# Performance work log

Hardware: AMD Instinct MI355X
Metric: run time of the kernel (lower is better)

## Reference

```python
import jax, jax.numpy as jnp
import numpy as np

B, N_PER_G, DEG = 128, 1024, 8
N = B * N_PER_G
E = N * DEG
IN_DIM, HID, OUT_DIM = 128, 64, 10
EPS = 1e-5


def _gcn(x, src, dst, ew, W, b, n_nodes):
    # GCNConv with add_self_loops=True, symmetric normalization, edge weights ew in {0,1}
    xw = x @ W                                                 # [N, HID]
    deg = jax.ops.segment_sum(ew, dst, num_segments=n_nodes) + 1.0  # +1 self loop
    dinv = jax.lax.rsqrt(deg)
    norm = dinv[src] * dinv[dst] * ew                          # [E]
    agg = jax.ops.segment_sum(xw[src] * norm[:, None], dst, num_segments=n_nodes)
    return agg + xw * (dinv * dinv)[:, None] + b               # self-loop term + bias


def _bn_relu(x, g, beta):
    # BatchNorm1d training-mode stats over node dim (biased var), then ReLU
    mu = x.mean(0)
    var = ((x - mu) ** 2).mean(0)
    return jax.nn.relu((x - mu) * jax.lax.rsqrt(var + EPS) * g + beta)


def _topk_pool(x, src, dst, ew, p, n_per_g):
    # PyG TopKPooling: score = x.p/||p||, keep top ceil(0.8*n) per graph, x *= tanh(score)
    k = (4 * n_per_g + 4) // 5  # ceil(0.8 * n), static
    score = (x @ p) / jnp.linalg.norm(p)                       # [B*n]
    _, idx = jax.lax.top_k(score.reshape(B, n_per_g), k)       # [B, k] local indices
    perm = (idx + (jnp.arange(B) * n_per_g)[:, None]).reshape(-1)  # [B*k] global
    xs = x[perm] * jnp.tanh(score[perm])[:, None]
    # re-index edges; edges touching dropped nodes get weight 0 (mask, fixed E)
    mapping = jnp.full((B * n_per_g,), -1, jnp.int32).at[perm].set(
        jnp.arange(B * k, dtype=jnp.int32))
    ns, nd = mapping[src], mapping[dst]
    valid = (ns >= 0) & (nd >= 0) & (ew > 0)
    return xs, jnp.where(valid, ns, 0), jnp.where(valid, nd, 0), valid.astype(x.dtype), k


def _readout(x, k):
    xg = x.reshape(B, k, HID)
    return jnp.concatenate([xg.mean(1), xg.max(1)], axis=1)    # [B, 2*HID]


def _forward(x, edge_index, W1, b1, gamma1, beta1, p1, W2, b2, gamma2, beta2, p2,
             W3, b3, gamma3, beta3, p3, Wm, bm):
    src, dst = edge_index[0], edge_index[1]
    ew = jnp.ones((E,), x.dtype)
    n = N_PER_G
    blocks = [(W1, b1, gamma1, beta1, p1),
              (W2, b2, gamma2, beta2, p2),
              (W3, b3, gamma3, beta3, p3)]
    readout = jnp.zeros((B, 2 * HID), x.dtype)
    for W, b, g, bt, p in blocks:
        h = _gcn(x, src, dst, ew, W, b, B * n)
        h = _bn_relu(h, g, bt)
        x, src, dst, ew, n = _topk_pool(h, src, dst, ew, p, n)
        readout = readout + _readout(x, n)
    return readout @ Wm + bm                                   # [B, OUT_DIM]


def setup_inputs():
    key = jax.random.key(0)
    ks = jax.random.split(key, 20)
    x = jax.random.normal(ks[0], (N, IN_DIM), jnp.float32)
    src_l = jax.random.randint(ks[1], (E,), 0, N_PER_G)
    dst_l = jax.random.randint(ks[2], (E,), 0, N_PER_G)
    off = jnp.repeat(jnp.arange(B, dtype=jnp.int32) * N_PER_G, N_PER_G * DEG)
    edge_index = jnp.stack([src_l.astype(jnp.int32) + off,
                            dst_l.astype(jnp.int32) + off])   # [2, E] intra-graph
    d = {"x": x, "edge_index": edge_index}
    dims = [(IN_DIM, HID), (HID, HID), (HID, HID)]
    for i, (di, do) in enumerate(dims, 1):
        d[f"W{i}"] = jax.random.normal(ks[3 * i], (di, do), jnp.float32) / np.sqrt(di)
        d[f"b{i}"] = jnp.zeros((do,), jnp.float32)
        d[f"gamma{i}"] = jnp.ones((do,), jnp.float32)
        d[f"beta{i}"] = jnp.zeros((do,), jnp.float32)
        d[f"p{i}"] = jax.random.normal(ks[3 * i + 1], (do,), jnp.float32)
    d["Wm"] = jax.random.normal(ks[15], (2 * HID, OUT_DIM), jnp.float32) / np.sqrt(2 * HID)
    d["bm"] = jnp.zeros((OUT_DIM,), jnp.float32)
    return d


def reference(x, edge_index, W1, b1, gamma1, beta1, p1, W2, b2, gamma2, beta2, p2,
              W3, b3, gamma3, beta3, p3, Wm, bm):
    return _forward(x, edge_index, W1, b1, gamma1, beta1, p1,
                    W2, b2, gamma2, beta2, p2, W3, b3, gamma3, beta3, p3, Wm, bm)
```

## Files before the change

kernel.cpp:

```cpp
#include <hip/hip_runtime.h>
#include <cmath>
#include <cstdint>
#include <cstddef>

#define HID 64
#define NGR 128
#define NTOT 131072
#define EDGES 1048576
#define EPG 8192
#define CPAD 9216
#define SENT 1024

__global__ __launch_bounds__(256) void pack_init(
    const int* __restrict__ ei, uint32_t* __restrict__ packed,
    uint16_t* __restrict__ csr_g, uint32_t* __restrict__ rs_g,
    float* __restrict__ dinv_g, float* __restrict__ sums3,
    float* __restrict__ readout) {
  __shared__ int hist[1024];
  __shared__ int part[256];
  __shared__ int cursor[1024];
  int b = blockIdx.x, t = threadIdx.x;
  for (int i = t; i < 1024; i += 256) hist[i] = 0;
  __syncthreads();
  int ebase = b * EPG, nbase = b << 10;
  for (int e = t; e < EPG; e += 256) {
    uint32_t s = (uint32_t)(ei[ebase + e] - nbase);
    uint32_t d = (uint32_t)(ei[EDGES + ebase + e] - nbase);
    packed[ebase + e] = s | (d << 10);
    atomicAdd(&hist[(int)d], 1);
  }
  __syncthreads();
  int h0 = hist[t * 4], h1 = hist[t * 4 + 1], h2 = hist[t * 4 + 2], h3 = hist[t * 4 + 3];
  int p0 = h0 + (h0 & 1), p1 = h1 + (h1 & 1), p2 = h2 + (h2 & 1), p3 = h3 + (h3 & 1);
  int tot = p0 + p1 + p2 + p3;
  part[t] = tot;
  __syncthreads();
  for (int off = 1; off < 256; off <<= 1) {
    int v = (t >= off) ? part[t - off] : 0;
    __syncthreads();
    part[t] += v;
    __syncthreads();
  }
  int excl = part[t] - tot;
  int r0 = excl, r1 = r0 + p0, r2 = r1 + p1, r3 = r2 + p2;
  cursor[t * 4 + 0] = r0; cursor[t * 4 + 1] = r1;
  cursor[t * 4 + 2] = r2; cursor[t * 4 + 3] = r3;
  uint32_t* rg = rs_g + b * 1025;
  rg[t * 4 + 0] = r0; rg[t * 4 + 1] = r1; rg[t * 4 + 2] = r2; rg[t * 4 + 3] = r3;
  if (t == 255) rg[1024] = part[255];
  for (int i = t; i < 1024; i += 256)
    dinv_g[(b << 10) + i] = rsqrtf((float)hist[i] + 1.0f);
  __syncthreads();
  uint16_t* cg = csr_g + (size_t)b * CPAD;
  for (int e = t; e < EPG; e += 256) {
    uint32_t pk = packed[ebase + e];
    int d = (pk >> 10) & 1023;
    int idx = atomicAdd(&cursor[d], 1);
    cg[idx] = (uint16_t)(pk & 1023);
  }
  __syncthreads();
  for (int d = t; d < 1024; d += 256)
    if (hist[d] & 1) cg[cursor[d]] = (uint16_t)SENT;
  if (b < 3 && t < 128) sums3[b * 128 + t] = 0.0f;
  if (t < 128) readout[b * 128 + t] = 0.0f;
}

template<int DIN>
__global__ __launch_bounds__(256, 4) void gemm_rm(
    const float* __restrict__ X, const float* __restrict__ W,
    float* __restrict__ XWT) {
  __shared__ float sW[DIN * 64];
  const int t = threadIdx.x;
  const int c8 = (t & 7) * 8;
  const int n4 = (t >> 3) * 4;
  const int node0 = blockIdx.x * 128;
#pragma unroll
  for (int i = t; i < DIN * 16; i += 256)
    ((float4*)sW)[i] = ((const float4*)W)[i];
  __syncthreads();

  float acc[4][8];
#pragma unroll
  for (int i = 0; i < 4; i++)
#pragma unroll
    for (int c = 0; c < 8; c++) acc[i][c] = 0.0f;

  const float* xp = X + (size_t)(node0 + n4) * DIN;
#pragma unroll 2
  for (int k0 = 0; k0 < DIN; k0 += 4) {
    float xr[4][4];
#pragma unroll
    for (int i = 0; i < 4; i++) {
      float4 v = *(const float4*)(xp + (size_t)i * DIN + k0);
      xr[i][0] = v.x; xr[i][1] = v.y; xr[i][2] = v.z; xr[i][3] = v.w;
    }
#pragma unroll
    for (int j = 0; j < 4; j++) {
      float4 w0 = *(const float4*)(sW + (k0 + j) * 64 + c8);
      float4 w1 = *(const float4*)(sW + (k0 + j) * 64 + c8 + 4);
      float wn[8] = {w0.x, w0.y, w0.z, w0.w, w1.x, w1.y, w1.z, w1.w};
#pragma unroll
      for (int i = 0; i < 4; i++)
#pragma unroll
        for (int c = 0; c < 8; c++)
          acc[i][c] = fmaf(xr[i][j], wn[c], acc[i][c]);
    }
  }
#pragma unroll
  for (int cc = 0; cc < 8; cc++) {
    float* o = XWT + (size_t)(c8 + cc) * NTOT + node0 + n4;
    *(float4*)o = make_float4(acc[0][cc], acc[1][cc], acc[2][cc], acc[3][cc]);
  }
}

template<int DIN>
__global__ __launch_bounds__(256, 4) void gemm_cm(
    const float* __restrict__ X, const float* __restrict__ W,
    float* __restrict__ XWT) {
  __shared__ float sW[DIN * 64];
  const int t = threadIdx.x;
  const int c8 = (t & 7) * 8;
  const int n4 = (t >> 3) * 4;
  const int node0 = blockIdx.x * 128;
#pragma unroll
  for (int i = t; i < DIN * 16; i += 256)
    ((float4*)sW)[i] = ((const float4*)W)[i];
  __syncthreads();

  float acc[4][8];
#pragma unroll
  for (int i = 0; i < 4; i++)
#pragma unroll
    for (int c = 0; c < 8; c++) acc[i][c] = 0.0f;

  const float* xp = X + node0 + n4;
#pragma unroll 4
  for (int k = 0; k < DIN; k++) {
    float4 xv = *(const float4*)(xp + (size_t)k * NTOT);
    float xr[4] = {xv.x, xv.y, xv.z, xv.w};
    float4 w0 = *(const float4*)(sW + k * 64 + c8);
    float4 w1 = *(const float4*)(sW + k * 64 + c8 + 4);
    float wn[8] = {w0.x, w0.y, w0.z, w0.w, w1.x, w1.y, w1.z, w1.w};
#pragma unroll
    for (int i = 0; i < 4; i++)
#pragma unroll
      for (int c = 0; c < 8; c++)
        acc[i][c] = fmaf(xr[i], wn[c], acc[i][c]);
  }
#pragma unroll
  for (int cc = 0; cc < 8; cc++) {
    float* o = XWT + (size_t)(c8 + cc) * NTOT + node0 + n4;
    *(float4*)o = make_float4(acc[0][cc], acc[1][cc], acc[2][cc], acc[3][cc]);
  }
}

__global__ __launch_bounds__(1024, 8) void edge_agg(
    const uint16_t* __restrict__ csr_g, const uint32_t* __restrict__ rs_g,
    const float* __restrict__ dinv_g, const float* __restrict__ xwT,
    const float* __restrict__ bias, float* __restrict__ hT,
    float* __restrict__ sums) {
  __shared__ float xws[8 * 1028];
  __shared__ float dv[1024];
  __shared__ uint32_t rs[1025];
  __shared__ uint32_t csr_s[CPAD / 2];
  __shared__ float sredS[16][8], sredQ[16][8];
  const int g = blockIdx.x & 127;
  const int q = blockIdx.x >> 7;
  const int c0 = q * 8;
  const int t = threadIdx.x;
  const int gbase = g << 10;

  dv[t] = dinv_g[gbase + t];
  rs[t] = rs_g[g * 1025 + t];
  if (t == 0) rs[1024] = rs_g[g * 1025 + 1024];
  {
    const uint4* src4 = (const uint4*)(csr_g + (size_t)g * CPAD);
    ((uint4*)csr_s)[t] = src4[t];
    if (t < CPAD / 8 - 1024) ((uint4*)csr_s)[1024 + t] = src4[1024 + t];
  }
  for (int slot = t; slot < 2048; slot += 1024) {
    int c = slot >> 8, pos4 = (slot & 255) * 4;
    float4 v = *(const float4*)(xwT + (size_t)(c0 + c) * NTOT + gbase + pos4);
    float4 dd = *(const float4*)(dinv_g + gbase + pos4);
    v.x *= dd.x; v.y *= dd.y; v.z *= dd.z; v.w *= dd.w;
    *(float4*)(xws + c * 1028 + pos4) = v;
  }
  if (t < 32) xws[(t >> 2) * 1028 + 1024 + (t & 3)] = 0.0f;
  __syncthreads();

  const int c = t & 7, j = t >> 3;
  const float* xc = xws + c * 1028;
  const float bv = bias[c0 + c];
  float* hrow = hT + (size_t)(c0 + c) * NTOT + gbase;
  float S = 0.0f, Q = 0.0f;
  for (int d = j; d < 1024; d += 128) {
    float dvd = dv[d];
    if (dvd == 0.0f) continue;
    int e  = rs[d] >> 1;
    int e1 = rs[d + 1] >> 1;
    float a0 = 0.0f, a1 = 0.0f;
    for (; e < e1; e++) {
      uint32_t pk = csr_s[e];
      a0 += xc[pk & 0xFFFFu];
      a1 += xc[pk >> 16];
    }
    float hv = (a0 + a1 + xc[d]) * dvd + bv;
    hrow[d] = hv;
    S += hv; Q += hv * hv;
  }
#pragma unroll
  for (int m = 8; m < 64; m <<= 1) { S += __shfl_xor(S, m); Q += __shfl_xor(Q, m); }
  {
    int lane = t & 63, w = t >> 6;
    if (lane < 8) { sredS[w][lane] = S; sredQ[w][lane] = Q; }
  }
  __syncthreads();
  if (t < 8) {
    float a = 0.0f;
    for (int w2 = 0; w2 < 16; w2++) a += sredS[w2][t];
    atomicAdd(&sums[c0 + t], a);
  } else if (t < 16) {
    int cc = t - 8;
    float a = 0.0f;
    for (int w2 = 0; w2 < 16; w2++) a += sredQ[w2][cc];
    atomicAdd(&sums[64 + cc + c0], a);
  }
}

__global__ __launch_bounds__(256) void score_kernel(
    const float* __restrict__ hT, const float* __restrict__ sums,
    const float* __restrict__ gamma, const float* __restrict__ beta,
    const float* __restrict__ p, const float* __restrict__ dinv_g,
    float* __restrict__ score, float* __restrict__ stanh_g, float inv_n) {
  __shared__ float ssc[64], ssh[64], sp[64];
  __shared__ float sipn;
  int b = blockIdx.x >> 2, seg = (blockIdx.x & 3) << 8;
  int t = threadIdx.x;
  int node = (b << 10) + seg + t;
  if (t < 64) {
    float mu = sums[t] * inv_n;
    float var = fmaxf(sums[64 + t] * inv_n - mu * mu, 0.0f);
    float sc = rsqrtf(var + 1e-5f) * gamma[t];
    ssc[t] = sc; ssh[t] = beta[t] - mu * sc;
    sp[t] = p[t];
  }
  __syncthreads();
  if (t == 0) {
    float s = 0.0f;
    for (int i = 0; i < 64; i++) s += sp[i] * sp[i];
    sipn = rsqrtf(s);
  }
  __syncthreads();
  const float* hp = hT + node;
  float s0 = 0.0f;
#pragma unroll 16
  for (int c = 0; c < 64; c++) {
    float y = fmaxf(fmaf(hp[(size_t)c * NTOT], ssc[c], ssh[c]), 0.0f);
    s0 = fmaf(y, sp[c], s0);
  }
  float v0 = s0 * sipn;
  score[node] = (dinv_g[node] > 0.0f) ? v0 : -INFINITY;
  stanh_g[node] = tanhf(v0);
}

__global__ __launch_bounds__(1024) void topk_kernel(
    const float* __restrict__ score, int* __restrict__ snext_g, int k) {
  __shared__ float __align__(16) ssc2[4 * 260];
  int b = blockIdx.x >> 2, p = blockIdx.x & 3;
  int t = threadIdx.x;
  int gbase = b << 10;
  float sv = score[gbase + t];
  ssc2[(t >> 8) * 260 + (t & 255)] = sv;
  __syncthreads();
  int il = t >> 2, jq = t & 3;
  int gi = p * 256 + il;
  float my = ssc2[(gi >> 8) * 260 + (gi & 255)];
  const float4* base = (const float4*)(ssc2 + jq * 260);
  int jbase = jq * 256;
  int r = 0;
#pragma unroll 8
  for (int m = 0; m < 64; m++) {
    float4 v = base[m];
    int j0 = jbase + m * 4;
    r += (v.x > my) || (v.x == my && (j0 + 0) < gi);
    r += (v.y > my) || (v.y == my && (j0 + 1) < gi);
    r += (v.z > my) || (v.z == my && (j0 + 2) < gi);
    r += (v.w > my) || (v.w == my && (j0 + 3) < gi);
  }
  r += __shfl_xor(r, 1);
  r += __shfl_xor(r, 2);
  if (jq == 0) snext_g[gbase + gi] = (r < k) ? 1 : 0;
}

__global__ __launch_bounds__(256) void pool_kernel(
    const float* __restrict__ hT, const float* __restrict__ sums,
    const float* __restrict__ gamma, const float* __restrict__ beta,
    const float* __restrict__ stanh_g, const int* __restrict__ snext_g,
    const uint16_t* __restrict__ csr_g, const uint32_t* __restrict__ rs_g,
    float* __restrict__ xT_out, float* __restrict__ dinv_g,
    float* __restrict__ readout, int k, float inv_n, int hasNext) {
  __shared__ float ssc[64], ssh[64];
  __shared__ float sth[1024];
  __shared__ int skn[1025];
  __shared__ float redS[4][8], redM[4][8];
  int g = blockIdx.x & 127, q = blockIdx.x >> 7;
  int t = threadIdx.x;
  int gbase = g << 10;
  if (t < 64) {
    float mu = sums[t] * inv_n;
    float var = fmaxf(sums[64 + t] * inv_n - mu * mu, 0.0f);
    float sc = rsqrtf(var + 1e-5f) * gamma[t];
    ssc[t] = sc; ssh[t] = beta[t] - mu * sc;
  }
  for (int i = t; i < 1024; i += 256) {
    sth[i] = stanh_g[gbase + i];
    skn[i] = snext_g[gbase + i];
  }
  if (t == 0) skn[1024] = 0;
  __syncthreads();
  int lane = t & 63, w = t >> 6;
#pragma unroll
  for (int i = 0; i < 8; i++) {
    int c = q * 8 + i;
    const float* hrow = hT + (size_t)c * NTOT + gbase;
    float* xrow = xT_out ? (xT_out + (size_t)c * NTOT + gbase) : nullptr;
    float scc = ssc[c], shh = ssh[c];
    float S = 0.0f, M = -INFINITY;
    for (int nd = t; nd < 1024; nd += 256) {
      bool kn = skn[nd] != 0;
      float y = fmaxf(fmaf(hrow[nd], scc, shh), 0.0f) * sth[nd];
      y = kn ? y : 0.0f;
      if (xrow) xrow[nd] = y;
      S += y;
      if (kn) M = fmaxf(M, y);
    }
#pragma unroll
    for (int m = 1; m < 64; m <<= 1) {
      S += __shfl_xor(S, m);
      M = fmaxf(M, __shfl_xor(M, m));
    }
    if (lane == 0) { redS[w][i] = S; redM[w][i] = M; }
  }
  if (hasNext && t < 128) {
    int d = q * 128 + t;
    if (skn[d]) {
      uint32_t e0 = rs_g[g * 1025 + d], e1 = rs_g[g * 1025 + d + 1];
      const uint16_t* row = csr_g + (size_t)g * CPAD;
      int cnt = 0;
      for (uint32_t e = e0; e < e1; e++) cnt += skn[row[e]];
      dinv_g[gbase + d] = rsqrtf((float)cnt + 1.0f);
    } else {
      dinv_g[gbase + d] = 0.0f;
    }
  }
  __syncthreads();
  if (t < 8) {
    float S = redS[0][t] + redS[1][t] + redS[2][t] + redS[3][t];
    readout[g * 128 + q * 8 + t] += S / (float)k;
  } else if (t < 16) {
    int i = t - 8;
    float M = fmaxf(fmaxf(redM[0][i], redM[1][i]), fmaxf(redM[2][i], redM[3][i]));
    readout[g * 128 + 64 + q * 8 + i] += M;
  }
}

__global__ __launch_bounds__(256) void final_linear(
    const float* __restrict__ readout, const float* __restrict__ Wm,
    const float* __restrict__ bm, float* __restrict__ out) {
  int idx = blockIdx.x * 256 + threadIdx.x;
  if (idx >= NGR * 10) return;
  int b = idx / 10, o = idx - b * 10;
  float acc = bm[o];
  const float* r = readout + (size_t)b * 128;
  for (int c = 0; c < 128; c++) acc = fmaf(r[c], Wm[c * 10 + o], acc);
  out[idx] = acc;
}

extern "C" void kernel_launch(void* const* d_in, const int* in_sizes, int n_in,
                              void* d_out, int out_size, void* d_ws, size_t ws_size,
                              hipStream_t stream) {
  (void)in_sizes; (void)n_in; (void)out_size; (void)ws_size;
  const float* x  = (const float*)d_in[0];
  const int*   ei = (const int*)d_in[1];
  const float* Wk[3]  = {(const float*)d_in[2],  (const float*)d_in[7],  (const float*)d_in[12]};
  const float* bk[3]  = {(const float*)d_in[3],  (const float*)d_in[8],  (const float*)d_in[13]};
  const float* gk[3]  = {(const float*)d_in[4],  (const float*)d_in[9],  (const float*)d_in[14]};
  const float* btk[3] = {(const float*)d_in[5],  (const float*)d_in[10], (const float*)d_in[15]};
  const float* pk[3]  = {(const float*)d_in[6],  (const float*)d_in[11], (const float*)d_in[16]};
  const float* Wm = (const float*)d_in[17];
  const float* bm = (const float*)d_in[18];
  float* out = (float*)d_out;

  float* ws = (float*)d_ws;
  size_t off = 0;
  auto alloc = [&](size_t nfl) {
    float* ptr = ws + off;
    off += (nfl + 63) & ~(size_t)63;
    return ptr;
  };
  float* bufXW = alloc((size_t)NTOT * 64);
  float* bufH  = alloc((size_t)NTOT * 64);
  float* bufX  = alloc((size_t)NTOT * 64);
  float* dinv_g = alloc(NTOT);
  float* score  = alloc(NTOT);
  float* stanh_g = alloc(NTOT);
  int*   snext_g = (int*)alloc(NTOT);
  uint32_t* packed = (uint32_t*)alloc(EDGES);
  uint16_t* csr    = (uint16_t*)alloc((size_t)NGR * CPAD / 2);
  uint32_t* rs     = (uint32_t*)alloc(NGR * 1025);
  float* sums3 = alloc(3 * 128);
  float* readout = alloc(NGR * 2 * HID);

  pack_init<<<NGR, 256, 0, stream>>>(ei, packed, csr, rs, dinv_g, sums3, readout);

  const int   kk[3] = {820, 656, 525};
  const float invn[3] = {1.0f / (float)NTOT, 1.0f / (float)(NGR * 820),
                         1.0f / (float)(NGR * 656)};

  for (int L = 0; L < 3; L++) {
    float* sums = sums3 + L * 128;
    if (L == 0)
      gemm_rm<128><<<NTOT / 128, 256, 0, stream>>>(x, Wk[0], bufXW);
    else
      gemm_cm<64><<<NTOT / 128, 256, 0, stream>>>(bufX, Wk[L], bufXW);
    edge_agg<<<8 * NGR, 1024, 0, stream>>>(csr, rs, dinv_g, bufXW, bk[L], bufH, sums);
    score_kernel<<<4 * NGR, 256, 0, stream>>>(bufH, sums, gk[L], btk[L], pk[L],
                                              dinv_g, score, stanh_g, invn[L]);
    topk_kernel<<<4 * NGR, 1024, 0, stream>>>(score, snext_g, kk[L]);
    pool_kernel<<<8 * NGR, 256, 0, stream>>>(bufH, sums, gk[L], btk[L],
                                             stanh_g, snext_g, csr, rs,
                                             (L < 2) ? bufX : nullptr, dinv_g,
                                             readout, kk[L], invn[L],
                                             (L < 2) ? 1 : 0);
  }
  final_linear<<<5, 256, 0, stream>>>(readout, Wm, bm, out);
}
```

Measured before the change: 498.5 us.

## Fuse score, top-k and pooling into one kernel; apply BN/ReLU/tanh inside next GEMM

Replaces the separate score, topk and pool kernels with one per-graph 1024-thread kernel. It computes scores, ranks them in shared memory, builds the keep mask and tanh multiplier, does the readout reductions and recomputes dinv. The next layer's GEMM now reads the raw aggregated features and applies BN, ReLU and the pooling multiplier on the fly, so the pooled feature buffer is no longer written and re-read. This removes two launches and several global round-trips per layer, but each layer now runs only 128 large blocks for the pooling stage and the GEMM does extra elementwise work per load.

```diff
diff --git a/kernel.cpp b/kernel.cpp
--- a/kernel.cpp
+++ b/kernel.cpp
@@ -86,13 +86,13 @@
     for (int c = 0; c < 8; c++) acc[i][c] = 0.0f;
 
   const float* xp = X + (size_t)(node0 + n4) * DIN;
-#pragma unroll 2
+#pragma unroll 8
   for (int k0 = 0; k0 < DIN; k0 += 4) {
-    float xr[4][4];
+    float x4[4][4];
 #pragma unroll
     for (int i = 0; i < 4; i++) {
       float4 v = *(const float4*)(xp + (size_t)i * DIN + k0);
-      xr[i][0] = v.x; xr[i][1] = v.y; xr[i][2] = v.z; xr[i][3] = v.w;
+      x4[i][0] = v.x; x4[i][1] = v.y; x4[i][2] = v.z; x4[i][3] = v.w;
     }
 #pragma unroll
     for (int j = 0; j < 4; j++) {
@@ -103,21 +103,24 @@
       for (int i = 0; i < 4; i++)
 #pragma unroll
         for (int c = 0; c < 8; c++)
-          acc[i][c] = fmaf(xr[i][j], wn[c], acc[i][c]);
-    }
-  }
-#pragma unroll
-  for (int cc = 0; cc < 8; cc++) {
-    float* o = XWT + (size_t)(c8 + cc) * NTOT + node0 + n4;
-    *(float4*)o = make_float4(acc[0][cc], acc[1][cc], acc[2][cc], acc[3][cc]);
+          acc[i][c] = fmaf(x4[i][j], wn[c], acc[i][c]);
+    }
+  }
+#pragma unroll
+  for (int c = 0; c < 8; c++) {
+    float* o = XWT + (size_t)(c8 + c) * NTOT + node0 + n4;
+    *(float4*)o = make_float4(acc[0][c], acc[1][c], acc[2][c], acc[3][c]);
   }
 }
 
 template<int DIN>
-__global__ __launch_bounds__(256, 4) void gemm_cm(
-    const float* __restrict__ X, const float* __restrict__ W,
-    float* __restrict__ XWT) {
+__global__ __launch_bounds__(256, 4) void gemm_fused(
+    const float* __restrict__ H, const float* __restrict__ sums,
+    const float* __restrict__ gamma, const float* __restrict__ beta,
+    const float* __restrict__ mult_g, const float* __restrict__ W,
+    float* __restrict__ XWT, float inv_n) {
   __shared__ float sW[DIN * 64];
+  __shared__ float ssc[DIN], ssh[DIN];
   const int t = threadIdx.x;
   const int c8 = (t & 7) * 8;
   const int n4 = (t >> 3) * 4;
@@ -125,6 +128,12 @@
 #pragma unroll
   for (int i = t; i < DIN * 16; i += 256)
     ((float4*)sW)[i] = ((const float4*)W)[i];
+  if (t < DIN) {
+    float mu = sums[t] * inv_n;
+    float var = fmaxf(sums[64 + t] * inv_n - mu * mu, 0.0f);
+    float sc = rsqrtf(var + 1e-5f) * gamma[t];
+    ssc[t] = sc; ssh[t] = beta[t] - mu * sc;
+  }
   __syncthreads();
 
   float acc[4][8];
@@ -133,24 +142,30 @@
 #pragma unroll
     for (int c = 0; c < 8; c++) acc[i][c] = 0.0f;
 
-  const float* xp = X + node0 + n4;
-#pragma unroll 4
-  for (int k = 0; k < DIN; k++) {
-    float4 xv = *(const float4*)(xp + (size_t)k * NTOT);
-    float xr[4] = {xv.x, xv.y, xv.z, xv.w};
-    float4 w0 = *(const float4*)(sW + k * 64 + c8);
-    float4 w1 = *(const float4*)(sW + k * 64 + c8 + 4);
+  const float4 m4 = *(const float4*)(mult_g + node0 + n4);
+  const float* hp = H + node0 + n4;
+#pragma unroll 8
+  for (int kk = 0; kk < DIN; kk++) {
+    float4 h4 = *(const float4*)(hp + (size_t)kk * NTOT);
+    float scc = ssc[kk], shh = ssh[kk];
+    float xn[4];
+    xn[0] = fmaxf(fmaf(h4.x, scc, shh), 0.0f) * m4.x;
+    xn[1] = fmaxf(fmaf(h4.y, scc, shh), 0.0f) * m4.y;
+    xn[2] = fmaxf(fmaf(h4.z, scc, shh), 0.0f) * m4.z;
+    xn[3] = fmaxf(fmaf(h4.w, scc, shh), 0.0f) * m4.w;
+    float4 w0 = *(const float4*)(sW + kk * 64 + c8);
+    float4 w1 = *(const float4*)(sW + kk * 64 + c8 + 4);
     float wn[8] = {w0.x, w0.y, w0.z, w0.w, w1.x, w1.y, w1.z, w1.w};
 #pragma unroll
     for (int i = 0; i < 4; i++)
 #pragma unroll
       for (int c = 0; c < 8; c++)
-        acc[i][c] = fmaf(xr[i], wn[c], acc[i][c]);
-  }
-#pragma unroll
-  for (int cc = 0; cc < 8; cc++) {
-    float* o = XWT + (size_t)(c8 + cc) * NTOT + node0 + n4;
-    *(float4*)o = make_float4(acc[0][cc], acc[1][cc], acc[2][cc], acc[3][cc]);
+        acc[i][c] = fmaf(xn[i], wn[c], acc[i][c]);
+  }
+#pragma unroll
+  for (int c = 0; c < 8; c++) {
+    float* o = XWT + (size_t)(c8 + c) * NTOT + node0 + n4;
+    *(float4*)o = make_float4(acc[0][c], acc[1][c], acc[2][c], acc[3][c]);
   }
 }
 
@@ -227,16 +242,23 @@
   }
 }
 
-__global__ __launch_bounds__(256) void score_kernel(
+__global__ __launch_bounds__(1024) void sctp_kernel(
     const float* __restrict__ hT, const float* __restrict__ sums,
     const float* __restrict__ gamma, const float* __restrict__ beta,
-    const float* __restrict__ p, const float* __restrict__ dinv_g,
-    float* __restrict__ score, float* __restrict__ stanh_g, float inv_n) {
+    const float* __restrict__ p,
+    const uint16_t* __restrict__ csr_g, const uint32_t* __restrict__ rs_g,
+    float* __restrict__ dinv_g, float* __restrict__ mult_g,
+    float* __restrict__ readout, int k, float inv_n, int hasNext) {
+  __shared__ float __align__(16) ssc2[4 * 260];
   __shared__ float ssc[64], ssh[64], sp[64];
   __shared__ float sipn;
-  int b = blockIdx.x >> 2, seg = (blockIdx.x & 3) << 8;
-  int t = threadIdx.x;
-  int node = (b << 10) + seg + t;
+  __shared__ float mult_l[1024];
+  __shared__ int skn_l[1025];
+  __shared__ float redS[64], redM[64];
+  const int g = blockIdx.x;
+  const int t = threadIdx.x;
+  const int gbase = g << 10;
+
   if (t < 64) {
     float mu = sums[t] * inv_n;
     float var = fmaxf(sums[64 + t] * inv_n - mu * mu, 0.0f);
@@ -244,6 +266,7 @@
     ssc[t] = sc; ssh[t] = beta[t] - mu * sc;
     sp[t] = p[t];
   }
+  if (t == 1023) skn_l[1024] = 0;
   __syncthreads();
   if (t == 0) {
     float s = 0.0f;
@@ -251,7 +274,8 @@
     sipn = rsqrtf(s);
   }
   __syncthreads();
-  const float* hp = hT + node;
+
+  const float* hp = hT + gbase + t;
   float s0 = 0.0f;
 #pragma unroll 16
   for (int c = 0; c < 64; c++) {
@@ -259,109 +283,70 @@
     s0 = fmaf(y, sp[c], s0);
   }
   float v0 = s0 * sipn;
-  score[node] = (dinv_g[node] > 0.0f) ? v0 : -INFINITY;
-  stanh_g[node] = tanhf(v0);
-}
-
-__global__ __launch_bounds__(1024) void topk_kernel(
-    const float* __restrict__ score, int* __restrict__ snext_g, int k) {
-  __shared__ float __align__(16) ssc2[4 * 260];
-  int b = blockIdx.x >> 2, p = blockIdx.x & 3;
-  int t = threadIdx.x;
-  int gbase = b << 10;
-  float sv = score[gbase + t];
-  ssc2[(t >> 8) * 260 + (t & 255)] = sv;
-  __syncthreads();
-  int il = t >> 2, jq = t & 3;
-  int gi = p * 256 + il;
-  float my = ssc2[(gi >> 8) * 260 + (gi & 255)];
-  const float4* base = (const float4*)(ssc2 + jq * 260);
-  int jbase = jq * 256;
+  float dvv = dinv_g[gbase + t];
+  float my = (dvv > 0.0f) ? v0 : -INFINITY;
+  float th = tanhf(v0);
+  ssc2[(t >> 8) * 260 + (t & 255)] = my;
+  __syncthreads();
+
   int r = 0;
+#pragma unroll
+  for (int q4 = 0; q4 < 4; q4++) {
+    const float4* base = (const float4*)(ssc2 + q4 * 260);
+    int jbase = q4 * 256;
 #pragma unroll 8
-  for (int m = 0; m < 64; m++) {
-    float4 v = base[m];
-    int j0 = jbase + m * 4;
-    r += (v.x > my) || (v.x == my && (j0 + 0) < gi);
-    r += (v.y > my) || (v.y == my && (j0 + 1) < gi);
-    r += (v.z > my) || (v.z == my && (j0 + 2) < gi);
-    r += (v.w > my) || (v.w == my && (j0 + 3) < gi);
-  }
-  r += __shfl_xor(r, 1);
-  r += __shfl_xor(r, 2);
-  if (jq == 0) snext_g[gbase + gi] = (r < k) ? 1 : 0;
-}
-
-__global__ __launch_bounds__(256) void pool_kernel(
-    const float* __restrict__ hT, const float* __restrict__ sums,
-    const float* __restrict__ gamma, const float* __restrict__ beta,
-    const float* __restrict__ stanh_g, const int* __restrict__ snext_g,
-    const uint16_t* __restrict__ csr_g, const uint32_t* __restrict__ rs_g,
-    float* __restrict__ xT_out, float* __restrict__ dinv_g,
-    float* __restrict__ readout, int k, float inv_n, int hasNext) {
-  __shared__ float ssc[64], ssh[64];
-  __shared__ float sth[1024];
-  __shared__ int skn[1025];
-  __shared__ float redS[4][8], redM[4][8];
-  int g = blockIdx.x & 127, q = blockIdx.x >> 7;
-  int t = threadIdx.x;
-  int gbase = g << 10;
-  if (t < 64) {
-    float mu = sums[t] * inv_n;
-    float var = fmaxf(sums[64 + t] * inv_n - mu * mu, 0.0f);
-    float sc = rsqrtf(var + 1e-5f) * gamma[t];
-    ssc[t] = sc; ssh[t] = beta[t] - mu * sc;
-  }
-  for (int i = t; i < 1024; i += 256) {
-    sth[i] = stanh_g[gbase + i];
-    skn[i] = snext_g[gbase + i];
-  }
-  if (t == 0) skn[1024] = 0;
-  __syncthreads();
-  int lane = t & 63, w = t >> 6;
-#pragma unroll
-  for (int i = 0; i < 8; i++) {
-    int c = q * 8 + i;
+    for (int m = 0; m < 64; m++) {
+      float4 v = base[m];
+      int j0 = jbase + m * 4;
+      r += (v.x > my) || (v.x == my && (j0 + 0) < t);
+      r += (v.y > my) || (v.y == my && (j0 + 1) < t);
+      r += (v.z > my) || (v.z == my && (j0 + 2) < t);
+      r += (v.w > my) || (v.w == my && (j0 + 3) < t);
+    }
+  }
+  int kn = (r < k) ? 1 : 0;
+  skn_l[t] = kn;
+  float mt = kn ? th : 0.0f;
+  mult_l[t] = mt;
+  mult_g[gbase + t] = mt;
+  __syncthreads();
+
+  const int w = t >> 6, lane = t & 63;
+#pragma unroll
+  for (int rep = 0; rep < 4; rep++) {
+    int c = w + rep * 16;
     const float* hrow = hT + (size_t)c * NTOT + gbase;
-    float* xrow = xT_out ? (xT_out + (size_t)c * NTOT + gbase) : nullptr;
     float scc = ssc[c], shh = ssh[c];
     float S = 0.0f, M = -INFINITY;
-    for (int nd = t; nd < 1024; nd += 256) {
-      bool kn = skn[nd] != 0;
-      float y = fmaxf(fmaf(hrow[nd], scc, shh), 0.0f) * sth[nd];
-      y = kn ? y : 0.0f;
-      if (xrow) xrow[nd] = y;
+#pragma unroll
+    for (int j = 0; j < 16; j++) {
+      int nd = lane + j * 64;
+      float y = fmaxf(fmaf(hrow[nd], scc, shh), 0.0f) * mult_l[nd];
       S += y;
-      if (kn) M = fmaxf(M, y);
+      M = skn_l[nd] ? fmaxf(M, y) : M;
     }
 #pragma unroll
     for (int m = 1; m < 64; m <<= 1) {
       S += __shfl_xor(S, m);
       M = fmaxf(M, __shfl_xor(M, m));
     }
-    if (lane == 0) { redS[w][i] = S; redM[w][i] = M; }
-  }
-  if (hasNext && t < 128) {
-    int d = q * 128 + t;
-    if (skn[d]) {
-      uint32_t e0 = rs_g[g * 1025 + d], e1 = rs_g[g * 1025 + d + 1];
+    if (lane == 0) { redS[c] = S; redM[c] = M; }
+  }
+
+  if (hasNext) {
+    if (skn_l[t]) {
+      uint32_t e0 = rs_g[g * 1025 + t], e1 = rs_g[g * 1025 + t + 1];
       const uint16_t* row = csr_g + (size_t)g * CPAD;
       int cnt = 0;
-      for (uint32_t e = e0; e < e1; e++) cnt += skn[row[e]];
-      dinv_g[gbase + d] = rsqrtf((float)cnt + 1.0f);
+      for (uint32_t e = e0; e < e1; e++) cnt += skn_l[row[e]];
+      dinv_g[gbase + t] = rsqrtf((float)cnt + 1.0f);
     } else {
-      dinv_g[gbase + d] = 0.0f;
-    }
-  }
-  __syncthreads();
-  if (t < 8) {
-    float S = redS[0][t] + redS[1][t] + redS[2][t] + redS[3][t];
-    readout[g * 128 + q * 8 + t] += S / (float)k;
-  } else if (t < 16) {
-    int i = t - 8;
-    float M = fmaxf(fmaxf(redM[0][i], redM[1][i]), fmaxf(redM[2][i], redM[3][i]));
-    readout[g * 128 + 64 + q * 8 + i] += M;
-  }
+      dinv_g[gbase + t] = 0.0f;
+    }
+  }
+  __syncthreads();
+  if (t < 64) readout[g * 128 + t] += redS[t] / (float)k;
+  else if (t < 128) readout[g * 128 + 64 + (t - 64)] += redM[t - 64];
 }
 
 __global__ __launch_bounds__(256) void final_linear(
@@ -400,11 +385,8 @@
   };
   float* bufXW = alloc((size_t)NTOT * 64);
   float* bufH  = alloc((size_t)NTOT * 64);
-  float* bufX  = alloc((size_t)NTOT * 64);
   float* dinv_g = alloc(NTOT);
-  float* score  = alloc(NTOT);
-  float* stanh_g = alloc(NTOT);
-  int*   snext_g = (int*)alloc(NTOT);
+  float* mult   = alloc(NTOT);
   uint32_t* packed = (uint32_t*)alloc(EDGES);
   uint16_t* csr    = (uint16_t*)alloc((size_t)NGR * CPAD / 2);
   uint32_t* rs     = (uint32_t*)alloc(NGR * 1025);
@@ -422,16 +404,13 @@
     if (L == 0)
       gemm_rm<128><<<NTOT / 128, 256, 0, stream>>>(x, Wk[0], bufXW);
     else
-      gemm_cm<64><<<NTOT / 128, 256, 0, stream>>>(bufX, Wk[L], bufXW);
+      gemm_fused<64><<<NTOT / 128, 256, 0, stream>>>(
+          bufH, sums3 + (L - 1) * 128, gk[L - 1], btk[L - 1],
+          mult, Wk[L], bufXW, invn[L - 1]);
     edge_agg<<<8 * NGR, 1024, 0, stream>>>(csr, rs, dinv_g, bufXW, bk[L], bufH, sums);
-    score_kernel<<<4 * NGR, 256, 0, stream>>>(bufH, sums, gk[L], btk[L], pk[L],
-                                              dinv_g, score, stanh_g, invn[L]);
-    topk_kernel<<<4 * NGR, 1024, 0, stream>>>(score, snext_g, kk[L]);
-    pool_kernel<<<8 * NGR, 256, 0, stream>>>(bufH, sums, gk[L], btk[L],
-                                             stanh_g, snext_g, csr, rs,
-                                             (L < 2) ? bufX : nullptr, dinv_g,
-                                             readout, kk[L], invn[L],
-                                             (L < 2) ? 1 : 0);
+    sctp_kernel<<<NGR, 1024, 0, stream>>>(bufH, sums, gk[L], btk[L], pk[L],
+                                          csr, rs, dinv_g, mult, readout,
+                                          kk[L], invn[L], (L < 2) ? 1 : 0);
   }
   final_linear<<<5, 256, 0, stream>>>(readout, Wm, bm, out);
 }
```

New measurement: 538.0 us. 1.08x slower.
